# Performance work log

Measured on AMD Instinct MI355X. Metric: run time of the kernel, lower is better.

## Reference

```python
import jax, jax.numpy as jnp
import numpy as np

N = 131072          # flattened ray-sample points
C = 32              # output_coordinate_dim per plane
BASE = 128          # base grid resolution
SCALES = [1, 2, 4]  # multiscale_res multipliers
HID = 256           # ResBlock / CondMLP hidden width
OUT = 16            # decoder output dim (geo features)
COMBS = [(0, 1), (0, 2), (1, 2)]  # itertools.combinations(range(3), 2)


def setup_inputs() -> dict:
    key = jax.random.key(0)
    ks = iter(jax.random.split(key, 64))
    inp = {}
    inp['pts'] = jax.random.uniform(next(ks), (N, 3), dtype=jnp.float32)
    inp['aabb'] = jnp.asarray([[0.0, 0.0, 0.0], [1.0, 1.0, 1.0]], dtype=jnp.float32)
    # 9 plane grids: 3 scales x 3 coordinate combinations, uniform in [0.1, 0.5)
    for s, mult in enumerate(SCALES):
        r = BASE * mult
        for ci in range(3):
            inp[f'plane_{s}_{ci}'] = jax.random.uniform(
                next(ks), (C, r, r), dtype=jnp.float32, minval=0.1, maxval=0.5)
    feat_dim = C * len(SCALES)  # concat across scales -> 96
    def lin(k, fin, fout):
        bound = 1.0 / np.sqrt(fin)
        kw, kb = jax.random.split(k)
        w = jax.random.uniform(kw, (fin, fout), dtype=jnp.float32, minval=-bound, maxval=bound)
        b = jax.random.uniform(kb, (fout,), dtype=jnp.float32, minval=-bound, maxval=bound)
        return w, b
    inp['l0_w'], inp['l0_b'] = lin(next(ks), feat_dim, HID)
    # 3 ResBlocks x 3 linears (lz, l1, l2), all 256x256 -> stacked
    rw, rb = [], []
    for _ in range(9):
        w, b = lin(next(ks), HID, HID)
        rw.append(w); rb.append(b)
    inp['res_w'] = jnp.stack(rw).reshape(3, 3, HID, HID)
    inp['res_b'] = jnp.stack(rb).reshape(3, 3, HID)
    inp['l1_w'], inp['l1_b'] = lin(next(ks), HID, OUT)
    return inp


def _bilinear(plane, xy):
    # plane: [C, H, W]; xy: [N, 2] in [-1, 1]; x -> W axis, y -> H axis
    # (F.grid_sample, align_corners=True; border clamp == zeros pad since pts in-bounds)
    Cc, H, W = plane.shape
    x = (xy[:, 0] + 1.0) * 0.5 * (W - 1)
    y = (xy[:, 1] + 1.0) * 0.5 * (H - 1)
    x0 = jnp.clip(jnp.floor(x), 0, W - 2).astype(jnp.int32)
    y0 = jnp.clip(jnp.floor(y), 0, H - 2).astype(jnp.int32)
    x1, y1 = x0 + 1, y0 + 1
    wx = (x - x0)[None, :]
    wy = (y - y0)[None, :]
    v = (plane[:, y0, x0] * (1 - wx) * (1 - wy)
         + plane[:, y0, x1] * wx * (1 - wy)
         + plane[:, y1, x0] * (1 - wx) * wy
         + plane[:, y1, x1] * wx * wy)          # [C, N]
    return v.T                                   # [N, C]


def _interp_ms(xn, planes):
    # planes: list of 3 scales, each a list of 3 [C,H,W] grids
    feats = []
    for scale_planes in planes:
        interp = 1.0
        for plane, (c0, c1) in zip(scale_planes, COMBS):
            xy = jnp.stack([xn[:, c0], xn[:, c1]], axis=-1)
            interp = interp * _bilinear(plane, xy)  # hadamard across planes
        feats.append(interp)
    return jnp.concatenate(feats, axis=-1)          # [N, C*num_scales]


def _cond_mlp(f, l0_w, l0_b, res_w, res_b, l1_w, l1_b):
    x = f @ l0_w + l0_b
    for i in range(3):
        z = jax.nn.relu(x @ res_w[i, 0] + res_b[i, 0])
        res = x + z
        x = jax.nn.relu(res @ res_w[i, 1] + res_b[i, 1])
        x = jax.nn.relu(x @ res_w[i, 2] + res_b[i, 2]) + res
    return jax.nn.sigmoid(x @ l1_w + l1_b)


def reference(pts, aabb,
              plane_0_0, plane_0_1, plane_0_2,
              plane_1_0, plane_1_1, plane_1_2,
              plane_2_0, plane_2_1, plane_2_2,
              l0_w, l0_b, res_w, res_b, l1_w, l1_b):
    xn = (pts - aabb[0]) * (2.0 / (aabb[1] - aabb[0])) - 1.0  # normalize_aabb
    planes = [[plane_0_0, plane_0_1, plane_0_2],
              [plane_1_0, plane_1_1, plane_1_2],
              [plane_2_0, plane_2_1, plane_2_2]]
    feats = _interp_ms(xn, planes)                            # [N, 96]
    return _cond_mlp(feats, l0_w, l0_b, res_w, res_b, l1_w, l1_b)  # [N, 16]
```

## Files before the change

### kernel.cpp

```cpp
#include <hip/hip_runtime.h>

typedef unsigned short u16;
typedef unsigned int u32;
typedef __attribute__((ext_vector_type(2))) unsigned int u32x2;
typedef __attribute__((ext_vector_type(4))) unsigned int u32x4;
typedef __attribute__((ext_vector_type(8))) short short8;
typedef __attribute__((ext_vector_type(8))) _Float16 half8;
typedef __attribute__((ext_vector_type(2))) __fp16 fp16x2;
typedef __attribute__((ext_vector_type(4))) float floatx4;

__device__ __forceinline__ u16 f2h(float f){ _Float16 h = (_Float16)f; return __builtin_bit_cast(u16, h); }
__device__ __forceinline__ u32 pkrtz(float a, float b){
  fp16x2 h = __builtin_amdgcn_cvt_pkrtz(a, b);
  return __builtin_bit_cast(u32, h);
}
__device__ __forceinline__ u32 pkmax0(u32 a){
  u32 d, z = 0;
  asm("v_pk_max_f16 %0, %1, %2" : "=v"(d) : "v"(a), "v"(z));
  return d;
}
__device__ __forceinline__ u32 pkadd(u32 a, u32 b){
  u32 d;
  asm("v_pk_add_f16 %0, %1, %2" : "=v"(d) : "v"(a), "v"(b));
  return d;
}
__device__ __forceinline__ u32 pkmul(u32 a, u32 b){
  u32 d;
  asm("v_pk_mul_f16 %0, %1, %2" : "=v"(d) : "v"(a), "v"(b));
  return d;
}
__device__ __forceinline__ u32 pkfma(u32 a, u32 b, u32 c){
  u32 d;
  asm("v_pk_fma_f16 %0, %1, %2, %3" : "=v"(d) : "v"(a), "v"(b), "v"(c));
  return d;
}

struct PlanePtrs { const void* p[9]; };
struct PrepArgs {
  const float* src[9]; u16* dst[9]; int blk0[10]; int HW[9];
  const float* l0_w; const float* res_w; const float* l1_w;
  u16* l0T; u16* resT; u16* l1T;
  int ptrans_blocks;
};

__device__ __forceinline__ void wconv_one(const float* src, u16* dst, int fin, int fout, int t){
  int per = fin * fout;
  int m = t / per, r = t - m*per;
  int KS = fin >> 5;
  int e = r & 7;
  int lane = (r >> 3) & 63;
  int fs = r >> 9;
  int ks = fs % KS, ft = fs / KS;
  int of = ft*16 + (lane & 15);
  int k  = ks*32 + (lane >> 4)*8 + e;
  dst[t] = f2h(src[(size_t)m*per + (size_t)k*fout + of]);
}

__global__ void prep_all_kernel(PrepArgs a){
  __shared__ float tile[32][257];
  int bi = blockIdx.x;
  if (bi < a.ptrans_blocks){
    int i = 0;
    #pragma unroll
    for (int k = 1; k < 9; k++) if (bi >= a.blk0[k]) i = k;
    const float* src = a.src[i];
    u16* dst = a.dst[i];
    const int HW = a.HW[i];
    const int t = threadIdx.x;
    const size_t hw0 = (size_t)(bi - a.blk0[i]) * 256;
    #pragma unroll
    for (int c = 0; c < 32; c++) tile[c][t] = src[(size_t)c*HW + hw0 + t];
    __syncthreads();
    u32* d32 = (u32*)(dst + hw0*32);
    #pragma unroll
    for (int k = 0; k < 16; k++){
      int idx = k*512 + t*2;
      int j = idx >> 5, cc = idx & 31;
      u32 lo = f2h(tile[cc][j]);
      u32 hi = f2h(tile[cc+1][j]);
      d32[k*256 + t] = lo | (hi << 16);
    }
  } else {
    int t = (bi - a.ptrans_blocks)*256 + threadIdx.x;
    if (t < 24576){ wconv_one(a.l0_w, a.l0T, 96, 256, t); return; }
    t -= 24576;
    if (t < 589824){ wconv_one(a.res_w, a.resT, 256, 256, t); return; }
    t -= 589824;
    if (t < 4096){ wconv_one(a.l1_w, a.l1T, 256, 16, t); }
  }
}

__global__ void interp_fb_kernel(const float* __restrict__ pts, const float* __restrict__ aabb,
                                 PlanePtrs pp, u16* __restrict__ feats, int N)
{
  int n = blockIdx.x*256 + threadIdx.x;
  if (n >= N) return;
  float xn[3];
  #pragma unroll
  for (int d=0; d<3; d++){
    float lo = aabb[d], hi = aabb[3+d];
    xn[d] = (pts[(size_t)n*3 + d] - lo) * (2.0f/(hi - lo)) - 1.0f;
  }
  const int c0s[3] = {0,0,1};
  const int c1s[3] = {1,2,2};
  #pragma unroll
  for (int s=0; s<3; s++){
    const int R = 128 << s;
    float prod[32];
    #pragma unroll
    for (int p=0; p<3; p++){
      float fx = (xn[c0s[p]] + 1.0f) * 0.5f * (float)(R-1);
      float fy = (xn[c1s[p]] + 1.0f) * 0.5f * (float)(R-1);
      float fx0 = fminf(fmaxf(floorf(fx), 0.0f), (float)(R-2));
      float fy0 = fminf(fmaxf(floorf(fy), 0.0f), (float)(R-2));
      int x0 = (int)fx0, y0 = (int)fy0;
      float wx = fx - fx0, wy = fy - fy0;
      float w00 = (1.0f-wx)*(1.0f-wy), w01 = wx*(1.0f-wy);
      float w10 = (1.0f-wx)*wy,        w11 = wx*wy;
      const size_t HW = (size_t)R*R;
      const float* b00f = (const float*)pp.p[s*3+p] + (size_t)y0*R + x0;
      #pragma unroll 4
      for (int c=0; c<32; c++){
        const float* q = b00f + (size_t)c*HW;
        float val = q[0]*w00 + q[1]*w01 + q[R]*w10 + q[R+1]*w11;
        prod[c] = (p == 0) ? val : prod[c]*val;
      }
    }
    #pragma unroll
    for (int vv=0; vv<4; vv++){
      short8 pk8;
      #pragma unroll
      for (int e=0; e<8; e++) pk8[e] = (short)f2h(prod[vv*8+e]);
      *(short8*)(feats + (size_t)n*96 + s*32 + vv*8) = pk8;
    }
  }
}

template<int KSTEPS>
__device__ __forceinline__ void mm_tile(const u16* X, const u16* __restrict__ WTs,
                                        int ftbase, int lane, floatx4 acc[4][4])
{
  const int lr = lane & 15, lg = lane >> 4;
  #pragma unroll 1
  for (int ks=0; ks<KSTEPS; ks++){
    half8 w[4];
    #pragma unroll
    for (int rf=0; rf<4; rf++)
      w[rf] = *(const half8*)(WTs + ((size_t)((ftbase+rf)*KSTEPS + ks)*64 + lane)*8);
    half8 x[4];
    #pragma unroll
    for (int cf=0; cf<4; cf++){
      int pt = cf*16 + lr;
      int byt = (pt*512 + (ks*32 + lg*8)*2) ^ ((pt & 31) << 4);
      x[cf] = *(const half8*)((const char*)X + byt);
    }
    __builtin_amdgcn_s_setprio(1);
    #pragma unroll
    for (int rf=0; rf<4; rf++)
      #pragma unroll
      for (int cf=0; cf<4; cf++)
        acc[rf][cf] = __builtin_amdgcn_mfma_f32_16x16x32_f16(w[rf], x[cf], acc[rf][cf], 0, 0, 0);
    __builtin_amdgcn_s_setprio(0);
  }
}

__device__ __forceinline__ void init_acc(const float* b, int wb, int lg, floatx4 acc[4][4]){
  #pragma unroll
  for (int rf=0; rf<4; rf++){
    float4 v = *(const float4*)(b + wb + rf*16 + lg*4);
    floatx4 bi = (floatx4){v.x, v.y, v.z, v.w};
    #pragma unroll
    for (int cf=0; cf<4; cf++) acc[rf][cf] = bi;
  }
}

template<int MODE>
__global__ __launch_bounds__(256, 3) void mlp_kernel(
    const float* __restrict__ pts, const float* __restrict__ aabb, PlanePtrs pp,
    const u16* __restrict__ feats,
    const u16* __restrict__ l0T, const u16* __restrict__ resT, const u16* __restrict__ l1T,
    const float* __restrict__ l0_b, const float* __restrict__ res_b, const float* __restrict__ l1_b,
    float* __restrict__ out)
{
  __shared__ u16 X[64*256];
  const int tid = threadIdx.x;
  const int wave = tid >> 6, lane = tid & 63;
  const int lr = lane & 15, lg = lane >> 4;
  const int n0 = blockIdx.x * 64;
  const int ftbase = wave * 4;
  const int wb = wave * 64;

  if constexpr (MODE == 1){
    const int pt = tid >> 2, v = tid & 3;
    const int n = n0 + pt;
    float xn[3];
    #pragma unroll
    for (int d=0; d<3; d++){
      float lo = aabb[d], hi = aabb[3+d];
      xn[d] = (pts[(size_t)n*3 + d] - lo) * (2.0f/(hi - lo)) - 1.0f;
    }
    const int c0s[3] = {0,0,1};
    const int c1s[3] = {1,2,2};
    #pragma unroll
    for (int s=0; s<3; s++){
      const int R = 128 << s;
      u32x4 prod;
      #pragma unroll
      for (int p=0; p<3; p++){
        float fx = (xn[c0s[p]] + 1.0f) * 0.5f * (float)(R-1);
        float fy = (xn[c1s[p]] + 1.0f) * 0.5f * (float)(R-1);
        float fx0 = fminf(fmaxf(floorf(fx), 0.0f), (float)(R-2));
        float fy0 = fminf(fmaxf(floorf(fy), 0.0f), (float)(R-2));
        int x0 = (int)fx0, y0 = (int)fy0;
        float wx = fx - fx0, wy = fy - fy0;
        u32 w00p = pkrtz((1.0f-wx)*(1.0f-wy), (1.0f-wx)*(1.0f-wy));
        u32 w01p = pkrtz(wx*(1.0f-wy),        wx*(1.0f-wy));
        u32 w10p = pkrtz((1.0f-wx)*wy,        (1.0f-wx)*wy);
        u32 w11p = pkrtz(wx*wy,               wx*wy);
        const u16* base = (const u16*)pp.p[s*3 + p];
        const u16* b00 = base + ((size_t)y0*R + x0)*32 + v*8;
        const u16* b10 = b00 + (size_t)R*32;
        u32x4 h00 = *(const u32x4*)b00;
        u32x4 h01 = *(const u32x4*)(b00 + 32);
        u32x4 h10 = *(const u32x4*)b10;
        u32x4 h11 = *(const u32x4*)(b10 + 32);
        #pragma unroll
        for (int i=0; i<4; i++){
          u32 a = pkmul(h00[i], w00p);
          a = pkfma(h01[i], w01p, a);
          a = pkfma(h10[i], w10p, a);
          a = pkfma(h11[i], w11p, a);
          prod[i] = (p == 0) ? a : pkmul(prod[i], a);
        }
      }
      int byt = (pt*512 + (s*32 + v*8)*2) ^ ((pt & 31) << 4);
      *(u32x4*)((char*)X + byt) = prod;
    }
  } else {
    #pragma unroll
    for (int i=0; i<3; i++){
      int id = tid + i*256;
      int row = id / 12, sub = id - row*12;
      short8 v = *(const short8*)(feats + (size_t)(n0+row)*96 + sub*8);
      int byt = (row*512 + sub*16) ^ ((row & 31) << 4);
      *(short8*)((char*)X + byt) = v;
    }
  }
  __syncthreads();

  floatx4 acc[4][4];
  u32 pk[4][4][2];

  init_acc(l0_b, wb, lg, acc);
  mm_tile<3>(X, l0T, ftbase, lane, acc);
  __syncthreads();
  #pragma unroll
  for (int rf=0; rf<4; rf++){
    int fby = (wb + rf*16 + lg*4)*2;
    #pragma unroll
    for (int cf=0; cf<4; cf++){
      int pt = cf*16 + lr;
      u32 p0 = pkrtz(acc[rf][cf][0], acc[rf][cf][1]);
      u32 p1 = pkrtz(acc[rf][cf][2], acc[rf][cf][3]);
      pk[rf][cf][0] = p0; pk[rf][cf][1] = p1;
      int byt = (pt*512 + fby) ^ ((pt & 31) << 4);
      *(u32x2*)((char*)X + byt) = (u32x2){p0, p1};
    }
  }
  __syncthreads();

  for (int rb=0; rb<3; rb++){
    const u16* W0 = resT + (size_t)(rb*3+0)*65536;
    const u16* W1 = resT + (size_t)(rb*3+1)*65536;
    const u16* W2 = resT + (size_t)(rb*3+2)*65536;
    const float* b0 = res_b + (rb*3+0)*256;
    const float* b1 = res_b + (rb*3+1)*256;
    const float* b2 = res_b + (rb*3+2)*256;

    init_acc(b0, wb, lg, acc);
    mm_tile<8>(X, W0, ftbase, lane, acc);
    __syncthreads();
    #pragma unroll
    for (int rf=0; rf<4; rf++){
      int fby = (wb + rf*16 + lg*4)*2;
      #pragma unroll
      for (int cf=0; cf<4; cf++){
        int pt = cf*16 + lr;
        u32 p0 = pkadd(pk[rf][cf][0], pkmax0(pkrtz(acc[rf][cf][0], acc[rf][cf][1])));
        u32 p1 = pkadd(pk[rf][cf][1], pkmax0(pkrtz(acc[rf][cf][2], acc[rf][cf][3])));
        pk[rf][cf][0] = p0; pk[rf][cf][1] = p1;
        int byt = (pt*512 + fby) ^ ((pt & 31) << 4);
        *(u32x2*)((char*)X + byt) = (u32x2){p0, p1};
      }
    }
    __syncthreads();

    init_acc(b1, wb, lg, acc);
    mm_tile<8>(X, W1, ftbase, lane, acc);
    __syncthreads();
    #pragma unroll
    for (int rf=0; rf<4; rf++){
      int fby = (wb + rf*16 + lg*4)*2;
      #pragma unroll
      for (int cf=0; cf<4; cf++){
        int pt = cf*16 + lr;
        u32 p0 = pkmax0(pkrtz(acc[rf][cf][0], acc[rf][cf][1]));
        u32 p1 = pkmax0(pkrtz(acc[rf][cf][2], acc[rf][cf][3]));
        int byt = (pt*512 + fby) ^ ((pt & 31) << 4);
        *(u32x2*)((char*)X + byt) = (u32x2){p0, p1};
      }
    }
    __syncthreads();

    init_acc(b2, wb, lg, acc);
    mm_tile<8>(X, W2, ftbase, lane, acc);
    __syncthreads();
    #pragma unroll
    for (int rf=0; rf<4; rf++){
      int fby = (wb + rf*16 + lg*4)*2;
      #pragma unroll
      for (int cf=0; cf<4; cf++){
        int pt = cf*16 + lr;
        u32 p0 = pkadd(pkmax0(pkrtz(acc[rf][cf][0], acc[rf][cf][1])), pk[rf][cf][0]);
        u32 p1 = pkadd(pkmax0(pkrtz(acc[rf][cf][2], acc[rf][cf][3])), pk[rf][cf][1]);
        pk[rf][cf][0] = p0; pk[rf][cf][1] = p1;
        int byt = (pt*512 + fby) ^ ((pt & 31) << 4);
        *(u32x2*)((char*)X + byt) = (u32x2){p0, p1};
      }
    }
    __syncthreads();
  }

  floatx4 accf;
  {
    float4 bo = *(const float4*)(l1_b + lg*4);
    accf = (floatx4){bo.x, bo.y, bo.z, bo.w};
  }
  #pragma unroll 1
  for (int ks=0; ks<8; ks++){
    int pt = wave*16 + lr;
    int byt = (pt*512 + (ks*32 + lg*8)*2) ^ ((pt&31)<<4);
    half8 x = *(const half8*)((const char*)X + byt);
    half8 w = *(const half8*)(l1T + ((size_t)ks*64 + lane)*8);
    accf = __builtin_amdgcn_mfma_f32_16x16x32_f16(w, x, accf, 0, 0, 0);
  }
  {
    int n_out = n0 + wave*16 + lr;
    float4 o;
    o.x = 1.0f / (1.0f + __expf(-accf[0]));
    o.y = 1.0f / (1.0f + __expf(-accf[1]));
    o.z = 1.0f / (1.0f + __expf(-accf[2]));
    o.w = 1.0f / (1.0f + __expf(-accf[3]));
    *(float4*)(out + (size_t)n_out*16 + lg*4) = o;
  }
}

extern "C" void kernel_launch(void* const* d_in, const int* in_sizes, int n_in,
                              void* d_out, int out_size, void* d_ws, size_t ws_size,
                              hipStream_t stream)
{
  const float* pts  = (const float*)d_in[0];
  const float* aabb = (const float*)d_in[1];
  const float* l0_w = (const float*)d_in[11];
  const float* res_w= (const float*)d_in[13];
  const float* l1_w = (const float*)d_in[15];
  const float* l0_b = (const float*)d_in[12];
  const float* res_b= (const float*)d_in[14];
  const float* l1_b = (const float*)d_in[16];
  const int N = in_sizes[0] / 3;

  char* ws = (char*)d_ws;
  const size_t woff_l0  = 0;
  const size_t woff_res = 49152;
  const size_t woff_l1  = woff_res + 9*65536*2;
  const size_t foff     = woff_l1 + 8192;
  const size_t poff     = foff + (size_t)N*96*2;

  static const int HWs[3] = {128*128, 256*256, 512*512};
  size_t pel[9]; size_t tot = 0;
  for (int s=0;s<3;s++) for (int p=0;p<3;p++){ pel[s*3+p] = tot; tot += (size_t)HWs[s]*32; }

  const bool tr_mode = (ws_size >= poff + tot*2);

  PlanePtrs pp;
  if (tr_mode){
    u16* pbase = (u16*)(ws + poff);
    PrepArgs pa;
    int b0 = 0;
    for (int i=0;i<9;i++){
      int s = i/3;
      pa.src[i] = (const float*)d_in[2+i];
      pa.dst[i] = pbase + pel[i];
      pa.blk0[i] = b0;
      pa.HW[i] = HWs[s];
      b0 += HWs[s]/256;
      pp.p[i] = pbase + pel[i];
    }
    pa.blk0[9] = b0;
    pa.ptrans_blocks = b0;
    pa.l0_w = l0_w; pa.res_w = res_w; pa.l1_w = l1_w;
    pa.l0T = (u16*)(ws+woff_l0); pa.resT = (u16*)(ws+woff_res); pa.l1T = (u16*)(ws+woff_l1);
    const int wconv_blocks = (24576+589824+4096+255)/256;
    prep_all_kernel<<<b0 + wconv_blocks, 256, 0, stream>>>(pa);

    mlp_kernel<1><<<N/64, 256, 0, stream>>>(pts, aabb, pp, (const u16*)nullptr,
        (const u16*)(ws+woff_l0), (const u16*)(ws+woff_res), (const u16*)(ws+woff_l1),
        l0_b, res_b, l1_b, (float*)d_out);
  } else {
    PrepArgs pa;
    for (int i=0;i<9;i++){ pa.src[i] = nullptr; pa.dst[i] = nullptr; pa.blk0[i] = 0; pa.HW[i] = HWs[i/3]; pp.p[i] = d_in[2+i]; }
    pa.blk0[9] = 0;
    pa.ptrans_blocks = 0;
    pa.l0_w = l0_w; pa.res_w = res_w; pa.l1_w = l1_w;
    pa.l0T = (u16*)(ws+woff_l0); pa.resT = (u16*)(ws+woff_res); pa.l1T = (u16*)(ws+woff_l1);
    const int wconv_blocks = (24576+589824+4096+255)/256;
    prep_all_kernel<<<wconv_blocks, 256, 0, stream>>>(pa);

    interp_fb_kernel<<<(N+255)/256, 256, 0, stream>>>(pts, aabb, pp, (u16*)(ws+foff), N);
    mlp_kernel<0><<<N/64, 256, 0, stream>>>(pts, aabb, pp, (const u16*)(ws+foff),
        (const u16*)(ws+woff_l0), (const u16*)(ws+woff_res), (const u16*)(ws+woff_l1),
        l0_b, res_b, l1_b, (float*)d_out);
  }
}
```

Measured before the change: 222.0 us.

## Switch MLP matmuls from 16x16x32 to 32x32x16 MFMA tiles

Replaces the 16x16x32 f16 MFMA tiling in the MLP layers with 32x32x16 MFMA, so each wave computes a 2x2 grid of 32x32 tiles instead of 4x4 of 16x16. The weight pre-transform is changed to match the new fragment layout, and the bias init and epilogue now follow the 32x32 accumulator layout. The aim is fewer MFMA issues and fewer operand loads per k-step, giving better operand reuse and throughput. In exchange there are twice as many k-steps, and LDS bank-conflict behaviour changes under the existing swizzle.

```diff
diff --git a/kernel.cpp b/kernel.cpp
--- a/kernel.cpp
+++ b/kernel.cpp
@@ -8,6 +8,7 @@
 typedef __attribute__((ext_vector_type(8))) _Float16 half8;
 typedef __attribute__((ext_vector_type(2))) __fp16 fp16x2;
 typedef __attribute__((ext_vector_type(4))) float floatx4;
+typedef __attribute__((ext_vector_type(16))) float floatx16;
 
 __device__ __forceinline__ u16 f2h(float f){ _Float16 h = (_Float16)f; return __builtin_bit_cast(u16, h); }
 __device__ __forceinline__ u32 pkrtz(float a, float b){
@@ -43,7 +44,7 @@
   int ptrans_blocks;
 };
 
-__device__ __forceinline__ void wconv_one(const float* src, u16* dst, int fin, int fout, int t){
+__device__ __forceinline__ void wconv_one16(const float* src, u16* dst, int fin, int fout, int t){
   int per = fin * fout;
   int m = t / per, r = t - m*per;
   int KS = fin >> 5;
@@ -55,6 +56,18 @@
   int k  = ks*32 + (lane >> 4)*8 + e;
   dst[t] = f2h(src[(size_t)m*per + (size_t)k*fout + of]);
 }
+__device__ __forceinline__ void wconv_one32(const float* src, u16* dst, int fin, int fout, int t){
+  int per = fin * fout;
+  int m = t / per, r = t - m*per;
+  int KS = fin >> 4;
+  int e = r & 7;
+  int lane = (r >> 3) & 63;
+  int fs = r >> 9;
+  int ks = fs % KS, ft = fs / KS;
+  int of = ft*32 + (lane & 31);
+  int k  = ks*16 + (lane >> 5)*8 + e;
+  dst[t] = f2h(src[(size_t)m*per + (size_t)k*fout + of]);
+}
 
 __global__ void prep_all_kernel(PrepArgs a){
   __shared__ float tile[32][257];
@@ -82,11 +95,11 @@
     }
   } else {
     int t = (bi - a.ptrans_blocks)*256 + threadIdx.x;
-    if (t < 24576){ wconv_one(a.l0_w, a.l0T, 96, 256, t); return; }
+    if (t < 24576){ wconv_one32(a.l0_w, a.l0T, 96, 256, t); return; }
     t -= 24576;
-    if (t < 589824){ wconv_one(a.res_w, a.resT, 256, 256, t); return; }
+    if (t < 589824){ wconv_one32(a.res_w, a.resT, 256, 256, t); return; }
     t -= 589824;
-    if (t < 4096){ wconv_one(a.l1_w, a.l1T, 256, 16, t); }
+    if (t < 4096){ wconv_one16(a.l1_w, a.l1T, 256, 16, t); }
   }
 }
 
@@ -137,40 +150,48 @@
 }
 
 template<int KSTEPS>
-__device__ __forceinline__ void mm_tile(const u16* X, const u16* __restrict__ WTs,
-                                        int ftbase, int lane, floatx4 acc[4][4])
+__device__ __forceinline__ void mm_tile32(const u16* X, const u16* __restrict__ WTs,
+                                          int ftbase2, int lane, floatx16 acc[2][2])
 {
-  const int lr = lane & 15, lg = lane >> 4;
+  const int lr5 = lane & 31, hg = lane >> 5;
   #pragma unroll 1
   for (int ks=0; ks<KSTEPS; ks++){
-    half8 w[4];
-    #pragma unroll
-    for (int rf=0; rf<4; rf++)
-      w[rf] = *(const half8*)(WTs + ((size_t)((ftbase+rf)*KSTEPS + ks)*64 + lane)*8);
-    half8 x[4];
-    #pragma unroll
-    for (int cf=0; cf<4; cf++){
-      int pt = cf*16 + lr;
-      int byt = (pt*512 + (ks*32 + lg*8)*2) ^ ((pt & 31) << 4);
+    half8 w[2];
+    #pragma unroll
+    for (int rf=0; rf<2; rf++)
+      w[rf] = *(const half8*)(WTs + ((size_t)((ftbase2+rf)*KSTEPS + ks)*64 + lane)*8);
+    half8 x[2];
+    #pragma unroll
+    for (int cf=0; cf<2; cf++){
+      int pt = cf*32 + lr5;
+      int byt = (pt*512 + (ks*16 + hg*8)*2) ^ ((pt & 31) << 4);
       x[cf] = *(const half8*)((const char*)X + byt);
     }
     __builtin_amdgcn_s_setprio(1);
     #pragma unroll
-    for (int rf=0; rf<4; rf++)
-      #pragma unroll
-      for (int cf=0; cf<4; cf++)
-        acc[rf][cf] = __builtin_amdgcn_mfma_f32_16x16x32_f16(w[rf], x[cf], acc[rf][cf], 0, 0, 0);
+    for (int rf=0; rf<2; rf++)
+      #pragma unroll
+      for (int cf=0; cf<2; cf++)
+        acc[rf][cf] = __builtin_amdgcn_mfma_f32_32x32x16_f16(w[rf], x[cf], acc[rf][cf], 0, 0, 0);
     __builtin_amdgcn_s_setprio(0);
   }
 }
 
-__device__ __forceinline__ void init_acc(const float* b, int wb, int lg, floatx4 acc[4][4]){
+__device__ __forceinline__ void init_acc32(const float* b, int wb, int hg, floatx16 acc[2][2]){
   #pragma unroll
-  for (int rf=0; rf<4; rf++){
-    float4 v = *(const float4*)(b + wb + rf*16 + lg*4);
-    floatx4 bi = (floatx4){v.x, v.y, v.z, v.w};
-    #pragma unroll
-    for (int cf=0; cf<4; cf++) acc[rf][cf] = bi;
+  for (int rf=0; rf<2; rf++){
+    int fb = wb + rf*32 + 4*hg;
+    #pragma unroll
+    for (int g=0; g<4; g++){
+      float4 v = *(const float4*)(b + fb + 8*g);
+      #pragma unroll
+      for (int cf=0; cf<2; cf++){
+        acc[rf][cf][4*g+0] = v.x;
+        acc[rf][cf][4*g+1] = v.y;
+        acc[rf][cf][4*g+2] = v.z;
+        acc[rf][cf][4*g+3] = v.w;
+      }
+    }
   }
 }
 
@@ -186,8 +207,9 @@
   const int tid = threadIdx.x;
   const int wave = tid >> 6, lane = tid & 63;
   const int lr = lane & 15, lg = lane >> 4;
+  const int lr5 = lane & 31, hg = lane >> 5;
   const int n0 = blockIdx.x * 64;
-  const int ftbase = wave * 4;
+  const int ftbase2 = wave * 2;
   const int wb = wave * 64;
 
   if constexpr (MODE == 1){
@@ -248,23 +270,26 @@
   }
   __syncthreads();
 
-  floatx4 acc[4][4];
-  u32 pk[4][4][2];
-
-  init_acc(l0_b, wb, lg, acc);
-  mm_tile<3>(X, l0T, ftbase, lane, acc);
+  floatx16 acc[2][2];
+  u32 pk[2][2][8];
+
+  init_acc32(l0_b, wb, hg, acc);
+  mm_tile32<6>(X, l0T, ftbase2, lane, acc);
   __syncthreads();
   #pragma unroll
-  for (int rf=0; rf<4; rf++){
-    int fby = (wb + rf*16 + lg*4)*2;
-    #pragma unroll
-    for (int cf=0; cf<4; cf++){
-      int pt = cf*16 + lr;
-      u32 p0 = pkrtz(acc[rf][cf][0], acc[rf][cf][1]);
-      u32 p1 = pkrtz(acc[rf][cf][2], acc[rf][cf][3]);
-      pk[rf][cf][0] = p0; pk[rf][cf][1] = p1;
-      int byt = (pt*512 + fby) ^ ((pt & 31) << 4);
-      *(u32x2*)((char*)X + byt) = (u32x2){p0, p1};
+  for (int rf=0; rf<2; rf++){
+    int fb = wb + rf*32 + 4*hg;
+    #pragma unroll
+    for (int cf=0; cf<2; cf++){
+      int pt = cf*32 + lr5;
+      #pragma unroll
+      for (int g=0; g<4; g++){
+        u32 p0 = pkrtz(acc[rf][cf][4*g+0], acc[rf][cf][4*g+1]);
+        u32 p1 = pkrtz(acc[rf][cf][4*g+2], acc[rf][cf][4*g+3]);
+        pk[rf][cf][2*g] = p0; pk[rf][cf][2*g+1] = p1;
+        int byt = (pt*512 + (fb + 8*g)*2) ^ ((pt & 31) << 4);
+        *(u32x2*)((char*)X + byt) = (u32x2){p0, p1};
+      }
     }
   }
   __syncthreads();
@@ -277,55 +302,64 @@
     const float* b1 = res_b + (rb*3+1)*256;
     const float* b2 = res_b + (rb*3+2)*256;
 
-    init_acc(b0, wb, lg, acc);
-    mm_tile<8>(X, W0, ftbase, lane, acc);
-    __syncthreads();
-    #pragma unroll
-    for (int rf=0; rf<4; rf++){
-      int fby = (wb + rf*16 + lg*4)*2;
-      #pragma unroll
-      for (int cf=0; cf<4; cf++){
-        int pt = cf*16 + lr;
-        u32 p0 = pkadd(pk[rf][cf][0], pkmax0(pkrtz(acc[rf][cf][0], acc[rf][cf][1])));
-        u32 p1 = pkadd(pk[rf][cf][1], pkmax0(pkrtz(acc[rf][cf][2], acc[rf][cf][3])));
-        pk[rf][cf][0] = p0; pk[rf][cf][1] = p1;
-        int byt = (pt*512 + fby) ^ ((pt & 31) << 4);
-        *(u32x2*)((char*)X + byt) = (u32x2){p0, p1};
-      }
-    }
-    __syncthreads();
-
-    init_acc(b1, wb, lg, acc);
-    mm_tile<8>(X, W1, ftbase, lane, acc);
-    __syncthreads();
-    #pragma unroll
-    for (int rf=0; rf<4; rf++){
-      int fby = (wb + rf*16 + lg*4)*2;
-      #pragma unroll
-      for (int cf=0; cf<4; cf++){
-        int pt = cf*16 + lr;
-        u32 p0 = pkmax0(pkrtz(acc[rf][cf][0], acc[rf][cf][1]));
-        u32 p1 = pkmax0(pkrtz(acc[rf][cf][2], acc[rf][cf][3]));
-        int byt = (pt*512 + fby) ^ ((pt & 31) << 4);
-        *(u32x2*)((char*)X + byt) = (u32x2){p0, p1};
-      }
-    }
-    __syncthreads();
-
-    init_acc(b2, wb, lg, acc);
-    mm_tile<8>(X, W2, ftbase, lane, acc);
-    __syncthreads();
-    #pragma unroll
-    for (int rf=0; rf<4; rf++){
-      int fby = (wb + rf*16 + lg*4)*2;
-      #pragma unroll
-      for (int cf=0; cf<4; cf++){
-        int pt = cf*16 + lr;
-        u32 p0 = pkadd(pkmax0(pkrtz(acc[rf][cf][0], acc[rf][cf][1])), pk[rf][cf][0]);
-        u32 p1 = pkadd(pkmax0(pkrtz(acc[rf][cf][2], acc[rf][cf][3])), pk[rf][cf][1]);
-        pk[rf][cf][0] = p0; pk[rf][cf][1] = p1;
-        int byt = (pt*512 + fby) ^ ((pt & 31) << 4);
-        *(u32x2*)((char*)X + byt) = (u32x2){p0, p1};
+    init_acc32(b0, wb, hg, acc);
+    mm_tile32<16>(X, W0, ftbase2, lane, acc);
+    __syncthreads();
+    #pragma unroll
+    for (int rf=0; rf<2; rf++){
+      int fb = wb + rf*32 + 4*hg;
+      #pragma unroll
+      for (int cf=0; cf<2; cf++){
+        int pt = cf*32 + lr5;
+        #pragma unroll
+        for (int g=0; g<4; g++){
+          u32 p0 = pkadd(pk[rf][cf][2*g],   pkmax0(pkrtz(acc[rf][cf][4*g+0], acc[rf][cf][4*g+1])));
+          u32 p1 = pkadd(pk[rf][cf][2*g+1], pkmax0(pkrtz(acc[rf][cf][4*g+2], acc[rf][cf][4*g+3])));
+          pk[rf][cf][2*g] = p0; pk[rf][cf][2*g+1] = p1;
+          int byt = (pt*512 + (fb + 8*g)*2) ^ ((pt & 31) << 4);
+          *(u32x2*)((char*)X + byt) = (u32x2){p0, p1};
+        }
+      }
+    }
+    __syncthreads();
+
+    init_acc32(b1, wb, hg, acc);
+    mm_tile32<16>(X, W1, ftbase2, lane, acc);
+    __syncthreads();
+    #pragma unroll
+    for (int rf=0; rf<2; rf++){
+      int fb = wb + rf*32 + 4*hg;
+      #pragma unroll
+      for (int cf=0; cf<2; cf++){
+        int pt = cf*32 + lr5;
+        #pragma unroll
+        for (int g=0; g<4; g++){
+          u32 p0 = pkmax0(pkrtz(acc[rf][cf][4*g+0], acc[rf][cf][4*g+1]));
+          u32 p1 = pkmax0(pkrtz(acc[rf][cf][4*g+2], acc[rf][cf][4*g+3]));
+          int byt = (pt*512 + (fb + 8*g)*2) ^ ((pt & 31) << 4);
+          *(u32x2*)((char*)X + byt) = (u32x2){p0, p1};
+        }
+      }
+    }
+    __syncthreads();
+
+    init_acc32(b2, wb, hg, acc);
+    mm_tile32<16>(X, W2, ftbase2, lane, acc);
+    __syncthreads();
+    #pragma unroll
+    for (int rf=0; rf<2; rf++){
+      int fb = wb + rf*32 + 4*hg;
+      #pragma unroll
+      for (int cf=0; cf<2; cf++){
+        int pt = cf*32 + lr5;
+        #pragma unroll
+        for (int g=0; g<4; g++){
+          u32 p0 = pkadd(pkmax0(pkrtz(acc[rf][cf][4*g+0], acc[rf][cf][4*g+1])), pk[rf][cf][2*g]);
+          u32 p1 = pkadd(pkmax0(pkrtz(acc[rf][cf][4*g+2], acc[rf][cf][4*g+3])), pk[rf][cf][2*g+1]);
+          pk[rf][cf][2*g] = p0; pk[rf][cf][2*g+1] = p1;
+          int byt = (pt*512 + (fb + 8*g)*2) ^ ((pt & 31) << 4);
+          *(u32x2*)((char*)X + byt) = (u32x2){p0, p1};
+        }
       }
     }
     __syncthreads();
```

New measurement: 252.2 us. 1.14x slower.
